# Kernel optimization log

Measured on AMD Instinct MI355X. Metric: run time of the kernel, lower is better.

Reference implementation:

```python
import jax, jax.numpy as jnp
import numpy as np

INPUT_DIM = 512
OUTPUT_DIM = 512
DEGREE = 7
ALPHA = 0.5


def setup_inputs() -> dict:
    key = jax.random.key(0)
    kx, kc = jax.random.split(key)
    x = jax.random.normal(kx, (8192, INPUT_DIM), dtype=jnp.float32)
    std = 1.0 / (INPUT_DIM * (DEGREE + 1))
    laguerre_coeffs = jax.random.normal(kc, (INPUT_DIM, OUTPUT_DIM, DEGREE + 1), dtype=jnp.float32) * std
    return {"x": x, "laguerre_coeffs": laguerre_coeffs}


def reference(x, laguerre_coeffs):
    # x: [B, I] -> tanh squashed
    xt = jnp.tanh(x.reshape(-1, INPUT_DIM))
    # Build Laguerre basis L_0..L_degree via the standard recurrence:
    # k*L_k = (2(k-1)+1+alpha - x)*L_{k-1} - (k-1+alpha)*L_{k-2}
    L0 = jnp.ones_like(xt)
    basis = [L0]
    if DEGREE > 0:
        L1 = 1.0 + ALPHA - xt
        basis.append(L1)
        Lkm2, Lkm1 = L0, L1
        for k in range(2, DEGREE + 1):
            Lk = ((2 * (k - 1) + 1 + ALPHA - xt) * Lkm1 - (k - 1 + ALPHA) * Lkm2) / k
            basis.append(Lk)
            Lkm2, Lkm1 = Lkm1, Lk
    laguerre = jnp.stack(basis, axis=-1)  # [B, I, D+1]
    y = jnp.einsum('bid,iod->bo', laguerre, laguerre_coeffs)
    return y
```

## Files before the change

### kernel.cpp

```cpp
#include <hip/hip_runtime.h>

#define B_ROWS 8192
#define IN_DIM 512
#define OUT_DIM 512
#define NDEG 8
#define KDIM (IN_DIM * NDEG)
#define ZSLICES 4
#define NKT 16

typedef short bf16x8 __attribute__((ext_vector_type(8)));
typedef float f32x4  __attribute__((ext_vector_type(4)));

__device__ __forceinline__ unsigned short f2bf(float f) {
  unsigned u = __float_as_uint(f);
  u += 0x7fffu + ((u >> 16) & 1u);
  return (unsigned short)(u >> 16);
}

__device__ __forceinline__ void laguerre8(float t, float* L) {
  L[0] = 1.0f;
  L[1] = 1.5f - t;
#pragma unroll
  for (int k = 2; k < NDEG; ++k)
    L[k] = ((2.0f * (float)k - 0.5f - t) * L[k - 1] -
            ((float)k - 0.5f) * L[k - 2]) * (1.0f / (float)k);
}


__global__ void prep_kernel(const float* __restrict__ x, const float* __restrict__ cf,
                            unsigned short* __restrict__ A, unsigned short* __restrict__ Bt) {
  int g = blockIdx.x;
  if (g < (B_ROWS * IN_DIM) / 256) {
    int idx = g * 256 + threadIdx.x;
    int b = idx >> 9, i = idx & 511;
    float L[NDEG];
    laguerre8(tanhf(x[idx]), L);
    uint4 v;
    v.x = (unsigned)f2bf(L[0]) | ((unsigned)f2bf(L[1]) << 16);
    v.y = (unsigned)f2bf(L[2]) | ((unsigned)f2bf(L[3]) << 16);
    v.z = (unsigned)f2bf(L[4]) | ((unsigned)f2bf(L[5]) << 16);
    v.w = (unsigned)f2bf(L[6]) | ((unsigned)f2bf(L[7]) << 16);
    int h = b >> 7, rb = b & 127, t = i >> 3, c = i & 7;
    size_t chunk = ((size_t)(h * 64 + t)) * 1024 + (rb >> 6) * 512 + (rb & 63) * 8 + (c ^ (rb & 7));
    ((uint4*)A)[chunk] = v;
  } else {
    int idx = (g - (B_ROWS * IN_DIM) / 256) * 256 + threadIdx.x;
    int i = idx >> 9, o = idx & 511;
    const float4* cp = (const float4*)(cf + (size_t)idx * 8);
    float4 c0 = cp[0], c1 = cp[1];
    uint4 v;
    v.x = (unsigned)f2bf(c0.x) | ((unsigned)f2bf(c0.y) << 16);
    v.y = (unsigned)f2bf(c0.z) | ((unsigned)f2bf(c0.w) << 16);
    v.z = (unsigned)f2bf(c1.x) | ((unsigned)f2bf(c1.y) << 16);
    v.w = (unsigned)f2bf(c1.z) | ((unsigned)f2bf(c1.w) << 16);
    int h = o >> 7, rb = o & 127, t = i >> 3, c = i & 7;
    size_t chunk = ((size_t)(h * 64 + t)) * 1024 + (rb >> 6) * 512 + (rb & 63) * 8 + (c ^ (rb & 7));
    ((uint4*)Bt)[chunk] = v;
  }
}


#define PH(buf, mq, ks, LOADBF, VMW, ...)                                          \
  {                                                                                \
    const unsigned short* Ab_ = lds + (buf)*16384 + wm*8192 + (mq)*4096 + arow*64; \
    _Pragma("unroll") for (int m4 = 0; m4 < 4; ++m4)                               \
      af[m4] = *(const bf16x8*)(Ab_ + m4*1024 + (e ^ ((ks)*32)));                  \
    if (LOADBF) {                                                                  \
      const unsigned short* Bb_ = lds + 32768 + (buf)*16384 + (wn>>1)*8192         \
                                  + (wn&1)*4096 + arow*64;                         \
      _Pragma("unroll") for (int ni = 0; ni < 4; ++ni)                             \
        bfr[ni] = *(const bf16x8*)(Bb_ + ni*1024 + (e ^ ((ks)*32)));               \
    }                                                                              \
    __VA_ARGS__;                                                                   \
    __builtin_amdgcn_s_barrier();                                                  \
    asm volatile("s_waitcnt lgkmcnt(0)" ::: "memory");                             \
    __builtin_amdgcn_sched_barrier(0);                                             \
    __builtin_amdgcn_s_setprio(1);                                                 \
    _Pragma("unroll") for (int m4 = 0; m4 < 4; ++m4)                               \
      _Pragma("unroll") for (int ni = 0; ni < 4; ++ni)                             \
        acc[(mq)*4+m4][ni] = __builtin_amdgcn_mfma_f32_16x16x32_bf16(              \
            af[m4], bfr[ni], acc[(mq)*4+m4][ni], 0, 0, 0);                         \
    __builtin_amdgcn_s_setprio(0);                                                 \
    if ((VMW) == 1) { asm volatile("s_waitcnt vmcnt(2)" ::: "memory");             \
                      __builtin_amdgcn_sched_barrier(0); }                         \
    if ((VMW) == 2) { asm volatile("s_waitcnt vmcnt(0)" ::: "memory");             \
                      __builtin_amdgcn_sched_barrier(0); }                         \
    __builtin_amdgcn_s_barrier();                                                  \
  }

__global__ __launch_bounds__(512, 2) void gemm_kernel(const unsigned short* __restrict__ A,
                                                      const unsigned short* __restrict__ Bt,
                                                      unsigned short* __restrict__ P) {
  __shared__ unsigned short lds[65536];

  const int tid = threadIdx.x;
  const int lane = tid & 63;
  const int w = tid >> 6;
  const int wm = w >> 2, wn = w & 3;

  const int g = blockIdx.x;
  const int j0 = g >> 3, xx = g & 7;
  const int My = ((j0 >> 3) << 3) | xx;
  const int n = (j0 >> 2) & 1;
  const int z = j0 & 3;

  const uint4* Ag = (const uint4*)A;
  const uint4* Bg = (const uint4*)Bt;

  const int arow = lane & 15, hi = lane >> 4;
  const int e = (hi ^ (arow & 7)) * 8;

  f32x4 zero = {0.f, 0.f, 0.f, 0.f};
  f32x4 acc[8][4];
#pragma unroll
  for (int mi = 0; mi < 8; ++mi)
#pragma unroll
    for (int ni = 0; ni < 4; ++ni) acc[mi][ni] = zero;

  auto STAGE_H = [&](int isB, int h, int tile, int buf) {
    const uint4* src = isB ? Bg : Ag;
    const int rowblk = (isB ? n * 2 : My * 2) + h;
    const size_t c0 = ((size_t)(rowblk * 64 + z * NKT + tile)) * 1024 + w * 64 + lane;
    unsigned short* d = lds + isB * 32768 + buf * 16384 + h * 8192 + w * 512;
    __builtin_amdgcn_global_load_lds(
        (const __attribute__((address_space(1))) unsigned int*)(src + c0),
        (__attribute__((address_space(3))) unsigned int*)d, 16, 0, 0);
    __builtin_amdgcn_global_load_lds(
        (const __attribute__((address_space(1))) unsigned int*)(src + c0 + 512),
        (__attribute__((address_space(3))) unsigned int*)(d + 4096), 16, 0, 0);
  };

  bf16x8 af[4], bfr[4];

  STAGE_H(0, 0, 0, 0); STAGE_H(0, 1, 0, 0);
  STAGE_H(1, 0, 0, 0); STAGE_H(1, 1, 0, 0);
  STAGE_H(1, 0, 1, 1);
  asm volatile("s_waitcnt vmcnt(2)" ::: "memory");
  __builtin_amdgcn_sched_barrier(0);
  __builtin_amdgcn_s_barrier();

  for (int it = 0; it < 7; ++it) {
    const int t1 = 2 * it + 1, t2 = 2 * it + 2, t3 = 2 * it + 3;
    PH(0, 0, 0, 1, 0, STAGE_H(1, 1, t1, 1));
    PH(0, 1, 0, 0, 0, STAGE_H(0, 0, t1, 1));
    PH(0, 0, 1, 1, 0, STAGE_H(0, 1, t1, 1));
    PH(0, 1, 1, 0, 1, STAGE_H(1, 0, t2, 0));
    PH(1, 0, 0, 1, 0, STAGE_H(0, 0, t2, 0));
    PH(1, 1, 0, 0, 0, STAGE_H(0, 1, t2, 0));
    PH(1, 0, 1, 1, 0, STAGE_H(1, 1, t2, 0));
    PH(1, 1, 1, 0, 1, STAGE_H(1, 0, t3, 1));
  }
  PH(0, 0, 0, 1, 0, STAGE_H(1, 1, 15, 1));
  PH(0, 1, 0, 0, 0, STAGE_H(0, 0, 15, 1));
  PH(0, 0, 1, 1, 0, STAGE_H(0, 1, 15, 1));
  PH(0, 1, 1, 0, 2, (void)0);
  PH(1, 0, 0, 1, 0, (void)0);
  PH(1, 1, 0, 0, 0, (void)0);
  PH(1, 0, 1, 1, 0, (void)0);
  PH(1, 1, 1, 0, 0, (void)0);

  unsigned short* W = lds + w * 8192;
#pragma unroll
  for (int mi = 0; mi < 8; ++mi)
#pragma unroll
    for (int ni = 0; ni < 4; ++ni) {
      int col = ni * 16 + arow;
      int c8 = col >> 3, cpos = col & 7;
#pragma unroll
      for (int r = 0; r < 4; ++r) {
        int row = mi * 16 + hi * 4 + r;
        W[row * 64 + ((c8 ^ (row & 7)) << 3) + cpos] = f2bf(acc[mi][ni][r]);
      }
    }
  const int rr = lane >> 3, cc = lane & 7;
#pragma unroll
  for (int it = 0; it < 16; ++it) {
    int row = it * 8 + rr;
    uint4 v = *(uint4*)&W[row * 64 + ((cc ^ (row & 7)) << 3)];
    size_t pr = ((size_t)z * B_ROWS + My * 256 + wm * 128 + row) * 512 + n * 256 + wn * 64 + cc * 8;
    *(uint4*)&P[pr] = v;
  }
}

__global__ void reduce_kernel(const unsigned short* __restrict__ P, float* __restrict__ out) {
  size_t t = (size_t)blockIdx.x * 256 + threadIdx.x;
  const uint4* p = (const uint4*)P;
  const size_t stride = (size_t)B_ROWS * OUT_DIM / 8;
  float s[8] = {0, 0, 0, 0, 0, 0, 0, 0};
#pragma unroll
  for (int zz = 0; zz < ZSLICES; ++zz) {
    uint4 v = p[t + zz * stride];
    unsigned q[4] = {v.x, v.y, v.z, v.w};
#pragma unroll
    for (int j = 0; j < 4; ++j) {
      s[2 * j]     += __uint_as_float((q[j] & 0xffffu) << 16);
      s[2 * j + 1] += __uint_as_float(q[j] & 0xffff0000u);
    }
  }
  float4 o0 = {s[0], s[1], s[2], s[3]}, o1 = {s[4], s[5], s[6], s[7]};
  ((float4*)out)[t * 2]     = o0;
  ((float4*)out)[t * 2 + 1] = o1;
}

__global__ void naive_kernel(const float* __restrict__ x, const float* __restrict__ c,
                             float* __restrict__ out) {
  __shared__ float bas[IN_DIM * NDEG];
  int b = blockIdx.x;
  for (int i = threadIdx.x; i < IN_DIM; i += 256) {
    float t = tanhf(x[(size_t)b * IN_DIM + i]);
    float L[NDEG];
    laguerre8(t, L);
#pragma unroll
    for (int d = 0; d < NDEG; ++d) bas[i * NDEG + d] = L[d];
  }
  __syncthreads();
  for (int o = threadIdx.x; o < OUT_DIM; o += 256) {
    float acc = 0.f;
    for (int i = 0; i < IN_DIM; ++i) {
      const float* cp = c + ((size_t)i * OUT_DIM + o) * NDEG;
#pragma unroll
      for (int d = 0; d < NDEG; ++d) acc += bas[i * NDEG + d] * cp[d];
    }
    out[(size_t)b * OUT_DIM + o] = acc;
  }
}

extern "C" void kernel_launch(void* const* d_in, const int* in_sizes, int n_in,
                              void* d_out, int out_size, void* d_ws, size_t ws_size,
                              hipStream_t stream) {
  const float* x    = (const float*)d_in[0];
  const float* coef = (const float*)d_in[1];
  float* out = (float*)d_out;

  const size_t A_BYTES  = (size_t)B_ROWS * KDIM * 2;
  const size_t P_BYTES  = (size_t)ZSLICES * B_ROWS * OUT_DIM * 2;
  const size_t BT_BYTES = (size_t)OUT_DIM * KDIM * 2;

  if (ws_size >= A_BYTES + P_BYTES + BT_BYTES) {
    unsigned short* Abuf = (unsigned short*)d_ws;
    unsigned short* Pp   = (unsigned short*)((char*)d_ws + A_BYTES);
    unsigned short* Bt   = (unsigned short*)((char*)d_ws + A_BYTES + P_BYTES);
    prep_kernel<<<(B_ROWS * IN_DIM + IN_DIM * OUT_DIM) / 256, 256, 0, stream>>>(x, coef, Abuf, Bt);
    gemm_kernel<<<256, 512, 0, stream>>>(Abuf, Bt, Pp);
    reduce_kernel<<<(B_ROWS * OUT_DIM / 8) / 256, 256, 0, stream>>>(Pp, out);
  } else {
    naive_kernel<<<B_ROWS, 256, 0, stream>>>(x, coef, out);
  }
}
```

Measured before the change: 67.10 us.

## Fuse tanh and Laguerre basis generation into GEMM, staging raw x via LDS

```diff
diff --git a/kernel.cpp b/kernel.cpp
--- a/kernel.cpp
+++ b/kernel.cpp
@@ -26,72 +26,107 @@
             ((float)k - 0.5f) * L[k - 2]) * (1.0f / (float)k);
 }
 
-
-__global__ void prep_kernel(const float* __restrict__ x, const float* __restrict__ cf,
-                            unsigned short* __restrict__ A, unsigned short* __restrict__ Bt) {
-  int g = blockIdx.x;
-  if (g < (B_ROWS * IN_DIM) / 256) {
-    int idx = g * 256 + threadIdx.x;
-    int b = idx >> 9, i = idx & 511;
-    float L[NDEG];
-    laguerre8(tanhf(x[idx]), L);
-    uint4 v;
-    v.x = (unsigned)f2bf(L[0]) | ((unsigned)f2bf(L[1]) << 16);
-    v.y = (unsigned)f2bf(L[2]) | ((unsigned)f2bf(L[3]) << 16);
-    v.z = (unsigned)f2bf(L[4]) | ((unsigned)f2bf(L[5]) << 16);
-    v.w = (unsigned)f2bf(L[6]) | ((unsigned)f2bf(L[7]) << 16);
-    int h = b >> 7, rb = b & 127, t = i >> 3, c = i & 7;
-    size_t chunk = ((size_t)(h * 64 + t)) * 1024 + (rb >> 6) * 512 + (rb & 63) * 8 + (c ^ (rb & 7));
-    ((uint4*)A)[chunk] = v;
-  } else {
-    int idx = (g - (B_ROWS * IN_DIM) / 256) * 256 + threadIdx.x;
-    int i = idx >> 9, o = idx & 511;
-    const float4* cp = (const float4*)(cf + (size_t)idx * 8);
-    float4 c0 = cp[0], c1 = cp[1];
-    uint4 v;
-    v.x = (unsigned)f2bf(c0.x) | ((unsigned)f2bf(c0.y) << 16);
-    v.y = (unsigned)f2bf(c0.z) | ((unsigned)f2bf(c0.w) << 16);
-    v.z = (unsigned)f2bf(c1.x) | ((unsigned)f2bf(c1.y) << 16);
-    v.w = (unsigned)f2bf(c1.z) | ((unsigned)f2bf(c1.w) << 16);
-    int h = o >> 7, rb = o & 127, t = i >> 3, c = i & 7;
-    size_t chunk = ((size_t)(h * 64 + t)) * 1024 + (rb >> 6) * 512 + (rb & 63) * 8 + (c ^ (rb & 7));
-    ((uint4*)Bt)[chunk] = v;
-  }
-}
-
-
-#define PH(buf, mq, ks, LOADBF, VMW, ...)                                          \
-  {                                                                                \
-    const unsigned short* Ab_ = lds + (buf)*16384 + wm*8192 + (mq)*4096 + arow*64; \
-    _Pragma("unroll") for (int m4 = 0; m4 < 4; ++m4)                               \
-      af[m4] = *(const bf16x8*)(Ab_ + m4*1024 + (e ^ ((ks)*32)));                  \
-    if (LOADBF) {                                                                  \
-      const unsigned short* Bb_ = lds + 32768 + (buf)*16384 + (wn>>1)*8192         \
-                                  + (wn&1)*4096 + arow*64;                         \
-      _Pragma("unroll") for (int ni = 0; ni < 4; ++ni)                             \
-        bfr[ni] = *(const bf16x8*)(Bb_ + ni*1024 + (e ^ ((ks)*32)));               \
-    }                                                                              \
-    __VA_ARGS__;                                                                   \
-    __builtin_amdgcn_s_barrier();                                                  \
-    asm volatile("s_waitcnt lgkmcnt(0)" ::: "memory");                             \
-    __builtin_amdgcn_sched_barrier(0);                                             \
-    __builtin_amdgcn_s_setprio(1);                                                 \
-    _Pragma("unroll") for (int m4 = 0; m4 < 4; ++m4)                               \
-      _Pragma("unroll") for (int ni = 0; ni < 4; ++ni)                             \
-        acc[(mq)*4+m4][ni] = __builtin_amdgcn_mfma_f32_16x16x32_bf16(              \
-            af[m4], bfr[ni], acc[(mq)*4+m4][ni], 0, 0, 0);                         \
-    __builtin_amdgcn_s_setprio(0);                                                 \
-    if ((VMW) == 1) { asm volatile("s_waitcnt vmcnt(2)" ::: "memory");             \
-                      __builtin_amdgcn_sched_barrier(0); }                         \
-    if ((VMW) == 2) { asm volatile("s_waitcnt vmcnt(0)" ::: "memory");             \
-                      __builtin_amdgcn_sched_barrier(0); }                         \
-    __builtin_amdgcn_s_barrier();                                                  \
-  }
-
-__global__ __launch_bounds__(512, 2) void gemm_kernel(const unsigned short* __restrict__ A,
+__device__ __forceinline__ float ftanh(float x) {
+  float e2 = __expf(2.0f * x);
+  return (e2 - 1.0f) * (1.0f / (e2 + 1.0f));
+}
+
+__device__ __forceinline__ uint4 bpack(float xv) {
+  float L[NDEG];
+  laguerre8(ftanh(xv), L);
+  uint4 v;
+  v.x = (unsigned)f2bf(L[0]) | ((unsigned)f2bf(L[1]) << 16);
+  v.y = (unsigned)f2bf(L[2]) | ((unsigned)f2bf(L[3]) << 16);
+  v.z = (unsigned)f2bf(L[4]) | ((unsigned)f2bf(L[5]) << 16);
+  v.w = (unsigned)f2bf(L[6]) | ((unsigned)f2bf(L[7]) << 16);
+  return v;
+}
+
+__global__ void prep_kernel(const float* __restrict__ cf, unsigned short* __restrict__ Bt) {
+  int idx = blockIdx.x * 256 + threadIdx.x;
+  int i = idx >> 9, o = idx & 511;
+  const float4* cp = (const float4*)(cf + (size_t)idx * 8);
+  float4 c0 = cp[0], c1 = cp[1];
+  uint4 v;
+  v.x = (unsigned)f2bf(c0.x) | ((unsigned)f2bf(c0.y) << 16);
+  v.y = (unsigned)f2bf(c0.z) | ((unsigned)f2bf(c0.w) << 16);
+  v.z = (unsigned)f2bf(c1.x) | ((unsigned)f2bf(c1.y) << 16);
+  v.w = (unsigned)f2bf(c1.z) | ((unsigned)f2bf(c1.w) << 16);
+  int h = o >> 7, rb = o & 127, t = i >> 3, c = i & 7;
+  size_t chunk = ((size_t)(h * 64 + t)) * 1024 + (rb >> 6) * 512 + (rb & 63) * 8 + (c ^ (rb & 7));
+  ((uint4*)Bt)[chunk] = v;
+}
+
+
+#define VM(N) { asm volatile("s_waitcnt vmcnt(" #N ")" ::: "memory");  \
+                __builtin_amdgcn_sched_barrier(0); }
+
+#define XSTAGE(tt, nb, h)                                                           \
+  {                                                                                 \
+    const float* xs = x + (size_t)(My * 256 + (h) * 128 + w * 16 + (lane >> 3)) * 512 \
+                        + (z * 16 + (tt)) * 8 + (lane & 7);                         \
+    unsigned short* xd = lds + 65536 + (nb) * 4096 + (h) * 2048 + w * 256;          \
+    __builtin_amdgcn_global_load_lds(                                               \
+        (const __attribute__((address_space(1))) unsigned int*)xs,                  \
+        (__attribute__((address_space(3))) unsigned int*)xd, 4, 0, 0);              \
+    __builtin_amdgcn_global_load_lds(                                               \
+        (const __attribute__((address_space(1))) unsigned int*)(xs + 8 * 512),      \
+        (__attribute__((address_space(3))) unsigned int*)(xd + 128), 4, 0, 0);      \
+  }
+
+#define BSTAGE(tt, nb, h)                                                           \
+  {                                                                                 \
+    const size_t c0_ = ((size_t)((n * 2 + (h)) * 64 + z * 16 + (tt))) * 1024        \
+                       + w * 64 + lane;                                             \
+    unsigned short* d_ = lds + 32768 + (nb) * 16384 + (h) * 8192 + w * 512;         \
+    __builtin_amdgcn_global_load_lds(                                               \
+        (const __attribute__((address_space(1))) unsigned int*)(Bg + c0_),          \
+        (__attribute__((address_space(3))) unsigned int*)d_, 16, 0, 0);             \
+    __builtin_amdgcn_global_load_lds(                                               \
+        (const __attribute__((address_space(1))) unsigned int*)(Bg + c0_ + 512),    \
+        (__attribute__((address_space(3))) unsigned int*)(d_ + 4096), 16, 0, 0);    \
+  }
+
+#define AC_HALF(nb, h)                                                              \
+  {                                                                                 \
+    float2 xv = *(const float2*)((const char*)lds + 131072 + (nb) * 8192            \
+                                 + (h) * 4096 + xoff);                              \
+    uint4 v0 = bpack(xv.x), v1 = bpack(xv.y);                                       \
+    unsigned short* dA = lds + (nb) * 16384 + (h) * 8192 + chkbase * 8;             \
+    *(uint4*)(dA + c0s * 8) = v0;                                                   \
+    *(uint4*)(dA + c1s * 8) = v1;                                                   \
+  }
+
+#define PHASE(AB, BB, MQ, KS, LOADBF, STAGE, POST)                                  \
+  {                                                                                 \
+    const unsigned short* Ab_ = lds + (AB) * 16384 + wm * 8192 + (MQ) * 4096        \
+                                + arow * 64;                                        \
+    _Pragma("unroll") for (int m4 = 0; m4 < 4; ++m4)                                \
+      af[m4] = *(const bf16x8*)(Ab_ + m4 * 1024 + (e ^ ((KS) * 32)));               \
+    if (LOADBF) {                                                                   \
+      const unsigned short* Bb_ = lds + 32768 + (BB) * 16384 + (wn >> 1) * 8192     \
+                                  + (wn & 1) * 4096 + arow * 64;                    \
+      _Pragma("unroll") for (int ni = 0; ni < 4; ++ni)                              \
+        bfr[ni] = *(const bf16x8*)(Bb_ + ni * 1024 + (e ^ ((KS) * 32)));            \
+    }                                                                               \
+    STAGE;                                                                          \
+    __builtin_amdgcn_s_barrier();                                                   \
+    asm volatile("s_waitcnt lgkmcnt(0)" ::: "memory");                              \
+    __builtin_amdgcn_sched_barrier(0);                                              \
+    __builtin_amdgcn_s_setprio(1);                                                  \
+    _Pragma("unroll") for (int m4 = 0; m4 < 4; ++m4)                                \
+      _Pragma("unroll") for (int ni = 0; ni < 4; ++ni)                              \
+        acc[(MQ) * 4 + m4][ni] = __builtin_amdgcn_mfma_f32_16x16x32_bf16(           \
+            af[m4], bfr[ni], acc[(MQ) * 4 + m4][ni], 0, 0, 0);                      \
+    __builtin_amdgcn_s_setprio(0);                                                  \
+    POST;                                                                           \
+    __builtin_amdgcn_s_barrier();                                                   \
+  }
+
+__global__ __launch_bounds__(512, 2) void gemm_kernel(const float* __restrict__ x,
                                                       const unsigned short* __restrict__ Bt,
                                                       unsigned short* __restrict__ P) {
-  __shared__ unsigned short lds[65536];
+  __shared__ __align__(16) unsigned short lds[73728];
 
   const int tid = threadIdx.x;
   const int lane = tid & 63;
@@ -104,12 +139,16 @@
   const int n = (j0 >> 2) & 1;
   const int z = j0 & 3;
 
-  const uint4* Ag = (const uint4*)A;
   const uint4* Bg = (const uint4*)Bt;
 
   const int arow = lane & 15, hi = lane >> 4;
   const int e = (hi ^ (arow & 7)) * 8;
 
+  const int rb = tid >> 2, ii0 = (tid & 3) * 2, sw = rb & 7;
+  const int chkbase = (rb >> 6) * 512 + (rb & 63) * 8;
+  const int c0s = ii0 ^ sw, c1s = (ii0 + 1) ^ sw;
+  const int xoff = (rb * 8 + ii0) * 4;
+
   f32x4 zero = {0.f, 0.f, 0.f, 0.f};
   f32x4 acc[8][4];
 #pragma unroll
@@ -117,47 +156,32 @@
 #pragma unroll
     for (int ni = 0; ni < 4; ++ni) acc[mi][ni] = zero;
 
-  auto STAGE_H = [&](int isB, int h, int tile, int buf) {
-    const uint4* src = isB ? Bg : Ag;
-    const int rowblk = (isB ? n * 2 : My * 2) + h;
-    const size_t c0 = ((size_t)(rowblk * 64 + z * NKT + tile)) * 1024 + w * 64 + lane;
-    unsigned short* d = lds + isB * 32768 + buf * 16384 + h * 8192 + w * 512;
-    __builtin_amdgcn_global_load_lds(
-        (const __attribute__((address_space(1))) unsigned int*)(src + c0),
-        (__attribute__((address_space(3))) unsigned int*)d, 16, 0, 0);
-    __builtin_amdgcn_global_load_lds(
-        (const __attribute__((address_space(1))) unsigned int*)(src + c0 + 512),
-        (__attribute__((address_space(3))) unsigned int*)(d + 4096), 16, 0, 0);
-  };
-
   bf16x8 af[4], bfr[4];
 
-  STAGE_H(0, 0, 0, 0); STAGE_H(0, 1, 0, 0);
-  STAGE_H(1, 0, 0, 0); STAGE_H(1, 1, 0, 0);
-  STAGE_H(1, 0, 1, 1);
-  asm volatile("s_waitcnt vmcnt(2)" ::: "memory");
-  __builtin_amdgcn_sched_barrier(0);
+  XSTAGE(0, 0, 0); XSTAGE(0, 0, 1);
+  BSTAGE(0, 0, 0); BSTAGE(0, 0, 1);
+  VM(4);
+  AC_HALF(0, 0); AC_HALF(0, 1);
+  asm volatile("s_waitcnt lgkmcnt(0)" ::: "memory");
+  VM(0);
   __builtin_amdgcn_s_barrier();
 
-  for (int it = 0; it < 7; ++it) {
-    const int t1 = 2 * it + 1, t2 = 2 * it + 2, t3 = 2 * it + 3;
-    PH(0, 0, 0, 1, 0, STAGE_H(1, 1, t1, 1));
-    PH(0, 1, 0, 0, 0, STAGE_H(0, 0, t1, 1));
-    PH(0, 0, 1, 1, 0, STAGE_H(0, 1, t1, 1));
-    PH(0, 1, 1, 0, 1, STAGE_H(1, 0, t2, 0));
-    PH(1, 0, 0, 1, 0, STAGE_H(0, 0, t2, 0));
-    PH(1, 1, 0, 0, 0, STAGE_H(0, 1, t2, 0));
-    PH(1, 0, 1, 1, 0, STAGE_H(1, 1, t2, 0));
-    PH(1, 1, 1, 0, 1, STAGE_H(1, 0, t3, 1));
-  }
-  PH(0, 0, 0, 1, 0, STAGE_H(1, 1, 15, 1));
-  PH(0, 1, 0, 0, 0, STAGE_H(0, 0, 15, 1));
-  PH(0, 0, 1, 1, 0, STAGE_H(0, 1, 15, 1));
-  PH(0, 1, 1, 0, 2, (void)0);
-  PH(1, 0, 0, 1, 0, (void)0);
-  PH(1, 1, 0, 0, 0, (void)0);
-  PH(1, 0, 1, 1, 0, (void)0);
-  PH(1, 1, 1, 0, 0, (void)0);
+#pragma unroll 1
+  for (int t = 0; t < NKT - 1; ++t) {
+    const int ct = t & 1, nb = ct ^ 1;
+    const int tt = t + 1;
+    PHASE(ct, ct, 0, 0, 1, { XSTAGE(tt, nb, 0); BSTAGE(tt, nb, 0); }, {});
+    PHASE(ct, ct, 1, 0, 0, { XSTAGE(tt, nb, 1); BSTAGE(tt, nb, 1); }, {});
+    PHASE(ct, ct, 0, 1, 1, {}, { VM(6); AC_HALF(nb, 0); });
+    PHASE(ct, ct, 1, 1, 0, {},
+          { VM(2); AC_HALF(nb, 1);
+            asm volatile("s_waitcnt lgkmcnt(0)" ::: "memory");
+            VM(0); });
+  }
+  PHASE(1, 1, 0, 0, 1, {}, {});
+  PHASE(1, 1, 1, 0, 0, {}, {});
+  PHASE(1, 1, 0, 1, 1, {}, {});
+  PHASE(1, 1, 1, 1, 0, {}, {});
 
   unsigned short* W = lds + w * 8192;
 #pragma unroll
@@ -232,16 +256,14 @@
   const float* coef = (const float*)d_in[1];
   float* out = (float*)d_out;
 
-  const size_t A_BYTES  = (size_t)B_ROWS * KDIM * 2;
   const size_t P_BYTES  = (size_t)ZSLICES * B_ROWS * OUT_DIM * 2;
   const size_t BT_BYTES = (size_t)OUT_DIM * KDIM * 2;
 
-  if (ws_size >= A_BYTES + P_BYTES + BT_BYTES) {
-    unsigned short* Abuf = (unsigned short*)d_ws;
-    unsigned short* Pp   = (unsigned short*)((char*)d_ws + A_BYTES);
-    unsigned short* Bt   = (unsigned short*)((char*)d_ws + A_BYTES + P_BYTES);
-    prep_kernel<<<(B_ROWS * IN_DIM + IN_DIM * OUT_DIM) / 256, 256, 0, stream>>>(x, coef, Abuf, Bt);
-    gemm_kernel<<<256, 512, 0, stream>>>(Abuf, Bt, Pp);
+  if (ws_size >= P_BYTES + BT_BYTES) {
+    unsigned short* Pp = (unsigned short*)d_ws;
+    unsigned short* Bt = (unsigned short*)((char*)d_ws + P_BYTES);
+    prep_kernel<<<(IN_DIM * OUT_DIM) / 256, 256, 0, stream>>>(coef, Bt);
+    gemm_kernel<<<256, 512, 0, stream>>>(x, Bt, Pp);
     reduce_kernel<<<(B_ROWS * OUT_DIM / 8) / 256, 256, 0, stream>>>(Pp, out);
   } else {
     naive_kernel<<<B_ROWS, 256, 0, stream>>>(x, coef, out);
```

Result: slower. 68.80 us (+2.5%).

## Fuse split-K reduction into GEMM via atomic tile counters; coalesce prep writes

Applied to the files above, without the earlier changes.

```diff
diff --git a/kernel.cpp b/kernel.cpp
--- a/kernel.cpp
+++ b/kernel.cpp
@@ -26,25 +26,40 @@
             ((float)k - 0.5f) * L[k - 2]) * (1.0f / (float)k);
 }
 
+__device__ __forceinline__ float ftanh(float x) {
+  float e2 = __expf(2.0f * x);
+  return (e2 - 1.0f) * (1.0f / (e2 + 1.0f));
+}
+
+__device__ __forceinline__ uint4 bpack(float xv) {
+  float L[NDEG];
+  laguerre8(ftanh(xv), L);
+  uint4 v;
+  v.x = (unsigned)f2bf(L[0]) | ((unsigned)f2bf(L[1]) << 16);
+  v.y = (unsigned)f2bf(L[2]) | ((unsigned)f2bf(L[3]) << 16);
+  v.z = (unsigned)f2bf(L[4]) | ((unsigned)f2bf(L[5]) << 16);
+  v.w = (unsigned)f2bf(L[6]) | ((unsigned)f2bf(L[7]) << 16);
+  return v;
+}
+
 
 __global__ void prep_kernel(const float* __restrict__ x, const float* __restrict__ cf,
-                            unsigned short* __restrict__ A, unsigned short* __restrict__ Bt) {
-  int g = blockIdx.x;
-  if (g < (B_ROWS * IN_DIM) / 256) {
-    int idx = g * 256 + threadIdx.x;
-    int b = idx >> 9, i = idx & 511;
-    float L[NDEG];
-    laguerre8(tanhf(x[idx]), L);
-    uint4 v;
-    v.x = (unsigned)f2bf(L[0]) | ((unsigned)f2bf(L[1]) << 16);
-    v.y = (unsigned)f2bf(L[2]) | ((unsigned)f2bf(L[3]) << 16);
-    v.z = (unsigned)f2bf(L[4]) | ((unsigned)f2bf(L[5]) << 16);
-    v.w = (unsigned)f2bf(L[6]) | ((unsigned)f2bf(L[7]) << 16);
-    int h = b >> 7, rb = b & 127, t = i >> 3, c = i & 7;
-    size_t chunk = ((size_t)(h * 64 + t)) * 1024 + (rb >> 6) * 512 + (rb & 63) * 8 + (c ^ (rb & 7));
-    ((uint4*)A)[chunk] = v;
-  } else {
-    int idx = (g - (B_ROWS * IN_DIM) / 256) * 256 + threadIdx.x;
+                            unsigned short* __restrict__ A, unsigned short* __restrict__ Bt,
+                            unsigned int* __restrict__ cnt) {
+  const int g = blockIdx.x, tid = threadIdx.x;
+  if (g < 4096) {
+    const int h = g >> 6, t = g & 63;
+    uint4* dst = (uint4*)A + (size_t)g * 1024;
+#pragma unroll
+    for (int q = 0; q < 4; ++q) {
+      int v = q * 256 + tid;
+      int rb = ((v >> 9) << 6) | ((v >> 3) & 63);
+      int c = (v & 7) ^ (rb & 7);
+      float xv = x[(size_t)(h * 128 + rb) * 512 + t * 8 + c];
+      dst[v] = bpack(xv);
+    }
+  } else if (g < 4096 + 1024) {
+    int idx = (g - 4096) * 256 + tid;
     int i = idx >> 9, o = idx & 511;
     const float4* cp = (const float4*)(cf + (size_t)idx * 8);
     float4 c0 = cp[0], c1 = cp[1];
@@ -56,9 +71,10 @@
     int h = o >> 7, rb = o & 127, t = i >> 3, c = i & 7;
     size_t chunk = ((size_t)(h * 64 + t)) * 1024 + (rb >> 6) * 512 + (rb & 63) * 8 + (c ^ (rb & 7));
     ((uint4*)Bt)[chunk] = v;
-  }
-}
-
+  } else {
+    if (tid < 64) cnt[tid] = 0;
+  }
+}
 
 #define PH(buf, mq, ks, LOADBF, VMW, ...)                                          \
   {                                                                                \
@@ -90,8 +106,11 @@
 
 __global__ __launch_bounds__(512, 2) void gemm_kernel(const unsigned short* __restrict__ A,
                                                       const unsigned short* __restrict__ Bt,
-                                                      unsigned short* __restrict__ P) {
+                                                      unsigned short* __restrict__ P,
+                                                      float* __restrict__ out,
+                                                      unsigned int* __restrict__ cnt) {
   __shared__ unsigned short lds[65536];
+  __shared__ int lastFlag;
 
   const int tid = threadIdx.x;
   const int lane = tid & 63;
@@ -180,26 +199,36 @@
     size_t pr = ((size_t)z * B_ROWS + My * 256 + wm * 128 + row) * 512 + n * 256 + wn * 64 + cc * 8;
     *(uint4*)&P[pr] = v;
   }
-}
-
-__global__ void reduce_kernel(const unsigned short* __restrict__ P, float* __restrict__ out) {
-  size_t t = (size_t)blockIdx.x * 256 + threadIdx.x;
-  const uint4* p = (const uint4*)P;
-  const size_t stride = (size_t)B_ROWS * OUT_DIM / 8;
-  float s[8] = {0, 0, 0, 0, 0, 0, 0, 0};
-#pragma unroll
-  for (int zz = 0; zz < ZSLICES; ++zz) {
-    uint4 v = p[t + zz * stride];
-    unsigned q[4] = {v.x, v.y, v.z, v.w};
-#pragma unroll
-    for (int j = 0; j < 4; ++j) {
-      s[2 * j]     += __uint_as_float((q[j] & 0xffffu) << 16);
-      s[2 * j + 1] += __uint_as_float(q[j] & 0xffff0000u);
-    }
-  }
-  float4 o0 = {s[0], s[1], s[2], s[3]}, o1 = {s[4], s[5], s[6], s[7]};
-  ((float4*)out)[t * 2]     = o0;
-  ((float4*)out)[t * 2 + 1] = o1;
+
+  __syncthreads();
+  __threadfence();
+  if (tid == 0)
+    lastFlag = ((int)atomicAdd(&cnt[My * 2 + n], 1u) == ZSLICES - 1);
+  __syncthreads();
+  if (lastFlag) {
+    __threadfence();
+    const size_t ss = (size_t)B_ROWS * OUT_DIM;
+#pragma unroll
+    for (int q = 0; q < 16; ++q) {
+      int el = q * 512 + tid;
+      int row = el >> 5, cc2 = el & 31;
+      size_t off = (size_t)(My * 256 + row) * 512 + n * 256 + cc2 * 8;
+      float s[8] = {0, 0, 0, 0, 0, 0, 0, 0};
+#pragma unroll
+      for (int zz = 0; zz < ZSLICES; ++zz) {
+        uint4 v = *(const uint4*)&P[off + zz * ss];
+        unsigned qv[4] = {v.x, v.y, v.z, v.w};
+#pragma unroll
+        for (int j = 0; j < 4; ++j) {
+          s[2 * j]     += __uint_as_float((qv[j] & 0xffffu) << 16);
+          s[2 * j + 1] += __uint_as_float(qv[j] & 0xffff0000u);
+        }
+      }
+      float4 f0 = {s[0], s[1], s[2], s[3]}, f1 = {s[4], s[5], s[6], s[7]};
+      *(float4*)&out[off]     = f0;
+      *(float4*)&out[off + 4] = f1;
+    }
+  }
 }
 
 __global__ void naive_kernel(const float* __restrict__ x, const float* __restrict__ c,
@@ -232,17 +261,17 @@
   const float* coef = (const float*)d_in[1];
   float* out = (float*)d_out;
 
-  const size_t A_BYTES  = (size_t)B_ROWS * KDIM * 2;
-  const size_t P_BYTES  = (size_t)ZSLICES * B_ROWS * OUT_DIM * 2;
-  const size_t BT_BYTES = (size_t)OUT_DIM * KDIM * 2;
-
-  if (ws_size >= A_BYTES + P_BYTES + BT_BYTES) {
+  const size_t A_B  = (size_t)B_ROWS * KDIM * 2;
+  const size_t P_B  = (size_t)ZSLICES * B_ROWS * OUT_DIM * 2;
+  const size_t BT_B = (size_t)OUT_DIM * KDIM * 2;
+
+  if (ws_size >= A_B + P_B + BT_B + 256) {
     unsigned short* Abuf = (unsigned short*)d_ws;
-    unsigned short* Pp   = (unsigned short*)((char*)d_ws + A_BYTES);
-    unsigned short* Bt   = (unsigned short*)((char*)d_ws + A_BYTES + P_BYTES);
-    prep_kernel<<<(B_ROWS * IN_DIM + IN_DIM * OUT_DIM) / 256, 256, 0, stream>>>(x, coef, Abuf, Bt);
-    gemm_kernel<<<256, 512, 0, stream>>>(Abuf, Bt, Pp);
-    reduce_kernel<<<(B_ROWS * OUT_DIM / 8) / 256, 256, 0, stream>>>(Pp, out);
+    unsigned short* Pp   = (unsigned short*)((char*)d_ws + A_B);
+    unsigned short* Bt   = (unsigned short*)((char*)d_ws + A_B + P_B);
+    unsigned int*   cnt  = (unsigned int*)((char*)d_ws + A_B + P_B + BT_B);
+    prep_kernel<<<4096 + 1024 + 1, 256, 0, stream>>>(x, coef, Abuf, Bt, cnt);
+    gemm_kernel<<<256, 512, 0, stream>>>(Abuf, Bt, Pp, out, cnt);
   } else {
     naive_kernel<<<B_ROWS, 256, 0, stream>>>(x, coef, out);
   }
```

Result: slower. 133.4 us (+98.8%).
